# Performance work log

Hardware: AMD Instinct MI355X
Metric: run time of the kernel (lower is better)

## Reference

```python
import jax, jax.numpy as jnp
import numpy as np

EPS_BN = 1e-5
EPS_LN = 1e-5


def _gcn_conv(x, W, b, src, dst, n_nodes):
    # PyG GCNConv: h = x @ W, add self-loops, symmetric deg^{-1/2} normalization,
    # scatter-add over edges, then + bias.
    h = x @ W                                            # [N, out]
    ones = jnp.ones(src.shape[0], dtype=h.dtype)
    deg = jax.ops.segment_sum(ones, dst, num_segments=n_nodes) + 1.0  # +1 for self-loop
    dinv = jax.lax.rsqrt(deg)                            # [N]
    coef = dinv[src] * dinv[dst]                         # [E]
    msg = h[src] * coef[:, None]                         # [E, out] gather + scale
    agg = jax.ops.segment_sum(msg, dst, num_segments=n_nodes)
    agg = agg + h * (dinv * dinv)[:, None]               # self-loop contribution
    return agg + b


def _encode(x, edge_index, W1, b1, bn_gamma, bn_beta, W2, b2, ln_gamma, ln_beta, lin_W, lin_b):
    n = x.shape[0]
    src, dst = edge_index[0], edge_index[1]
    h = _gcn_conv(x, W1, b1, src, dst, n)
    # BatchNorm1d (training mode: batch statistics over nodes, biased var)
    mu = jnp.mean(h, axis=0)
    var = jnp.mean((h - mu) ** 2, axis=0)
    h = (h - mu) * jax.lax.rsqrt(var + EPS_BN) * bn_gamma + bn_beta
    h = jax.nn.relu(h)
    h = _gcn_conv(h, W2, b2, src, dst, n)
    # LayerNorm over feature dim
    mu2 = jnp.mean(h, axis=-1, keepdims=True)
    var2 = jnp.mean((h - mu2) ** 2, axis=-1, keepdims=True)
    h = (h - mu2) * jax.lax.rsqrt(var2 + EPS_LN) * ln_gamma + ln_beta
    h = jax.nn.relu(h)
    return h @ lin_W + lin_b


def setup_inputs() -> dict:
    key = jax.random.key(0)
    ks = jax.random.split(key, 16)
    N, E, EL = 100000, 800000, 200000
    C_in, C_hid, C_out = 128, 256, 128
    inp = {}
    inp["x"] = jax.random.normal(ks[0], (N, C_in), dtype=jnp.float32)
    inp["edge_index"] = jax.random.randint(ks[1], (2, E), 0, N, dtype=jnp.int64)
    inp["edge_label_index"] = jax.random.randint(ks[2], (2, EL), 0, N, dtype=jnp.int64)
    inp["cutoff"] = jnp.zeros((), dtype=jnp.float32)
    s1 = 1.0 / np.sqrt(C_in)
    s2 = 1.0 / np.sqrt(C_hid)
    s3 = 1.0 / np.sqrt(C_out)
    inp["W1"] = jax.random.uniform(ks[3], (C_in, C_hid), jnp.float32, -s1, s1)
    inp["b1"] = jnp.zeros((C_hid,), jnp.float32)
    inp["bn_gamma"] = jnp.ones((C_hid,), jnp.float32)
    inp["bn_beta"] = jnp.zeros((C_hid,), jnp.float32)
    inp["W2"] = jax.random.uniform(ks[4], (C_hid, C_out), jnp.float32, -s2, s2)
    inp["b2"] = jnp.zeros((C_out,), jnp.float32)
    inp["ln_gamma"] = jnp.ones((C_out,), jnp.float32)
    inp["ln_beta"] = jnp.zeros((C_out,), jnp.float32)
    inp["lin_W"] = jax.random.uniform(ks[5], (C_out, C_out), jnp.float32, -s3, s3)
    inp["lin_b"] = jax.random.uniform(ks[6], (C_out,), jnp.float32, -s3, s3)
    return inp


def reference(x, edge_index, edge_label_index, cutoff, W1, b1, bn_gamma, bn_beta, W2, b2, ln_gamma, ln_beta, lin_W, lin_b):
    z = _encode(x, edge_index, W1, b1, bn_gamma, bn_beta, W2, b2, ln_gamma, ln_beta, lin_W, lin_b)
    # decode: per-pair dot product + thresholding
    edge_values = jnp.sum(z[edge_label_index[0]] * z[edge_label_index[1]], axis=-1)  # [EL]
    rounded = jnp.where(edge_values < cutoff, jnp.zeros_like(edge_values), jnp.ones_like(edge_values))
    return edge_values, jax.lax.stop_gradient(rounded)
```

## Files before the change

### kernel.cpp

```cpp
#include <hip/hip_runtime.h>
#include <stdint.h>


#define C_IN  128
#define C_HID 256
#define C_OUT 128
#define SCAN_B 256

typedef __attribute__((ext_vector_type(8))) short bf16x8;
typedef __attribute__((ext_vector_type(4))) float f32x4;

__device__ __forceinline__ short f2bf(float f) {
  union { float f; uint32_t u; } v; v.f = f;
  uint32_t r = v.u + 0x7FFFu + ((v.u >> 16) & 1u);
  return (short)(r >> 16);
}
__device__ __forceinline__ uint32_t pack_bf2(float a, float b) {
  return (uint32_t)(uint16_t)f2bf(a) | ((uint32_t)(uint16_t)f2bf(b) << 16);
}
__device__ __forceinline__ float bflo(uint32_t p) {
  union { uint32_t u; float f; } v; v.u = p << 16; return v.f;
}
__device__ __forceinline__ float bfhi(uint32_t p) {
  union { uint32_t u; float f; } v; v.u = p & 0xffff0000u; return v.f;
}
__device__ __forceinline__ float bfs(short s) {
  union { uint32_t u; float f; } v; v.u = ((uint32_t)(uint16_t)s) << 16; return v.f;
}

__device__ __forceinline__ void acc8(float* a, uint4 p, float w) {
  a[0] += bflo(p.x) * w; a[1] += bfhi(p.x) * w;
  a[2] += bflo(p.y) * w; a[3] += bfhi(p.y) * w;
  a[4] += bflo(p.z) * w; a[5] += bfhi(p.z) * w;
  a[6] += bflo(p.w) * w; a[7] += bfhi(p.w) * w;
}

__device__ __forceinline__ void async_cp16(const void* g, void* l) {
  __builtin_amdgcn_global_load_lds((const __attribute__((address_space(1))) void*)g,
                                   (__attribute__((address_space(3))) void*)l, 16, 0, 0);
}


__global__ __launch_bounds__(256) void hist_kernel(const int* __restrict__ dst,
                                                   int* __restrict__ counts,
                                                   int* __restrict__ ofs, int E) {
  int e = blockIdx.x * 256 + threadIdx.x;
  if (e < E) ofs[e] = atomicAdd(&counts[dst[e]], 1);
}

__global__ __launch_bounds__(256) void scan_part(const int* __restrict__ counts,
                                                 int* __restrict__ blockSums,
                                                 float* __restrict__ dinv,
                                                 int n, int per) {
  __shared__ int ws[4];
  int b = blockIdx.x;
  int start = b * per, end = min(n, start + per);
  int s = 0;
  for (int i = start + threadIdx.x; i < end; i += 256) {
    int c = counts[i];
    s += c;
    dinv[i] = rsqrtf((float)c + 1.0f);
  }
#pragma unroll
  for (int d = 1; d < 64; d <<= 1) s += __shfl_xor(s, d);
  if ((threadIdx.x & 63) == 0) ws[threadIdx.x >> 6] = s;
  __syncthreads();
  if (threadIdx.x == 0) blockSums[b] = ws[0] + ws[1] + ws[2] + ws[3];
}

__global__ __launch_bounds__(256) void scan_final(const int* __restrict__ counts,
                                                  const int* __restrict__ blockSums,
                                                  int* __restrict__ row_ptr,
                                                  int n, int per) {
  __shared__ int wsum[4];
  __shared__ int sbase;
  int tid = threadIdx.x, lane = tid & 63, wid = tid >> 6;
  int b = blockIdx.x;
  {
    int v = (tid < b) ? blockSums[tid] : 0;
#pragma unroll
    for (int d = 1; d < 64; d <<= 1) v += __shfl_xor(v, d);
    if (lane == 0) wsum[wid] = v;
    __syncthreads();
    if (tid == 0) sbase = wsum[0] + wsum[1] + wsum[2] + wsum[3];
    __syncthreads();
  }
  int start = b * per, end = min(n + 1, start + per);
  for (int chunk = start; chunk < end; chunk += 256) {
    int idx = chunk + tid;
    int v = (idx < n) ? counts[idx] : 0;
    int x = v;
#pragma unroll
    for (int d = 1; d < 64; d <<= 1) {
      int y = __shfl_up(x, d, 64);
      if (lane >= d) x += y;
    }
    if (lane == 63) wsum[wid] = x;
    __syncthreads();
    if (tid == 0) {
      int run = sbase;
#pragma unroll
      for (int w = 0; w < 4; ++w) { int t = wsum[w]; wsum[w] = run; run += t; }
      sbase = run;
    }
    __syncthreads();
    if (idx < end) row_ptr[idx] = wsum[wid] + x - v;
    __syncthreads();
  }
}

__global__ __launch_bounds__(256) void place_kernel(const int* __restrict__ src,
                                                    const int* __restrict__ dst,
                                                    const int* __restrict__ row_ptr,
                                                    const int* __restrict__ ofs,
                                                    const float* __restrict__ dinv,
                                                    int2* __restrict__ edges, int E) {
  int e = blockIdx.x * 256 + threadIdx.x;
  if (e < E) {
    int d = dst[e], s = src[e];
    int pos = row_ptr[d] + ofs[e];
    int2 ed; ed.x = s; ed.y = __float_as_int(dinv[s] * dinv[d]);
    edges[pos] = ed;
  }
}


__global__ __launch_bounds__(256) void cvt_all(const float* __restrict__ x,
                                               short* __restrict__ x_bf, int n4,
                                               const float* __restrict__ W1,
                                               short* __restrict__ w1t,
                                               const float* __restrict__ W2,
                                               short* __restrict__ w2t,
                                               const float* __restrict__ W3,
                                               short* __restrict__ w3t) {
  int i = blockIdx.x * 256 + threadIdx.x;
  if (i < n4) {
    float4 v = ((const float4*)x)[i];
    short4 o;
    o.x = f2bf(v.x); o.y = f2bf(v.y); o.z = f2bf(v.z); o.w = f2bf(v.w);
    ((short4*)x_bf)[i] = o;
    return;
  }
  int j = i - n4;
  if (j < 32768) {
    int k = j >> 8, n = j & 255;
    w1t[n * 128 + k] = f2bf(W1[j]);
  } else if (j < 65536) {
    int jj = j - 32768; int k = jj >> 7, n = jj & 127;
    w2t[n * 256 + k] = f2bf(W2[jj]);
  } else if (j < 81920) {
    int jj = j - 65536; int k = jj >> 7, n = jj & 127;
    w3t[n * 128 + k] = f2bf(W3[jj]);
  }
}


template <int MODE>
__global__ __launch_bounds__(256, 2) void bgemm_big(const short* __restrict__ A,
                                                    const short* __restrict__ BT,
                                                    const float* __restrict__ bias,
                                                    short* __restrict__ Cout,
                                                    float* __restrict__ pS,
                                                    float* __restrict__ pSS,
                                                    const float* __restrict__ bnp,
                                                    int M, int N, int K) {
  __shared__ short smem[2 * 128 * 128];
  short* As = smem;
  short* Bs = smem + 128 * 128;
  const int tid = threadIdx.x;
  const int w = tid >> 6, lane = tid & 63;
  const int wM = w >> 1, wN = w & 1;
  const int rowBase = blockIdx.y * 128;
  const int colBase = blockIdx.x * 128;
  const int l15 = lane & 15, q = lane >> 4;

  f32x4 acc[4][4];
#pragma unroll
  for (int i = 0; i < 4; ++i)
#pragma unroll
    for (int j = 0; j < 4; ++j) acc[i][j] = (f32x4){0.f, 0.f, 0.f, 0.f};

  for (int k0 = 0; k0 < K; k0 += 128) {
    if (MODE == 3) {
#pragma unroll
      for (int it = 0; it < 8; ++it) {
        int p = it * 256 + tid;
        int row = p >> 4, kcp = p & 15;
        int kc = kcp ^ (row & 15);
        int gm = rowBase + row; if (gm >= M) gm = M - 1;
        int c = k0 + kc * 8;
        bf16x8 av = *(const bf16x8*)&A[(size_t)gm * K + c];
        float4 s0 = *(const float4*)&bnp[c];
        float4 s1 = *(const float4*)&bnp[c + 4];
        float4 h0 = *(const float4*)&bnp[K + c];
        float4 h1 = *(const float4*)&bnp[K + c + 4];
        short res[8];
        res[0] = f2bf(fmaxf(bfs(av[0]) * s0.x + h0.x, 0.f));
        res[1] = f2bf(fmaxf(bfs(av[1]) * s0.y + h0.y, 0.f));
        res[2] = f2bf(fmaxf(bfs(av[2]) * s0.z + h0.z, 0.f));
        res[3] = f2bf(fmaxf(bfs(av[3]) * s0.w + h0.w, 0.f));
        res[4] = f2bf(fmaxf(bfs(av[4]) * s1.x + h1.x, 0.f));
        res[5] = f2bf(fmaxf(bfs(av[5]) * s1.y + h1.y, 0.f));
        res[6] = f2bf(fmaxf(bfs(av[6]) * s1.z + h1.z, 0.f));
        res[7] = f2bf(fmaxf(bfs(av[7]) * s1.w + h1.w, 0.f));
        bf16x8 rv;
#pragma unroll
        for (int j = 0; j < 8; ++j) rv[j] = res[j];
        *(bf16x8*)&As[p * 8] = rv;
      }
    } else {
#pragma unroll
      for (int it = 0; it < 8; ++it) {
        int p = it * 256 + tid;
        int row = p >> 4, kcp = p & 15;
        int kc = kcp ^ (row & 15);
        int gm = rowBase + row; if (gm >= M) gm = M - 1;
        async_cp16(A + (size_t)gm * K + k0 + kc * 8, &As[(it * 256 + w * 64) * 8]);
      }
    }
#pragma unroll
    for (int it = 0; it < 8; ++it) {
      int p = it * 256 + tid;
      int row = p >> 4, kcp = p & 15;
      int kc = kcp ^ (row & 15);
      async_cp16(BT + (size_t)(colBase + row) * K + k0 + kc * 8,
                 &Bs[(it * 256 + w * 64) * 8]);
    }
    __syncthreads();

#pragma unroll
    for (int ks = 0; ks < 4; ++ks) {
      bf16x8 af[4], bfr[4];
#pragma unroll
      for (int tm = 0; tm < 4; ++tm) {
        int row = wM * 64 + tm * 16 + l15;
        int kcp = (ks * 4 + q) ^ l15;
        af[tm] = *(const bf16x8*)&As[(row * 16 + kcp) * 8];
      }
#pragma unroll
      for (int tn = 0; tn < 4; ++tn) {
        int row = wN * 64 + tn * 16 + l15;
        int kcp = (ks * 4 + q) ^ l15;
        bfr[tn] = *(const bf16x8*)&Bs[(row * 16 + kcp) * 8];
      }
#pragma unroll
      for (int tm = 0; tm < 4; ++tm)
#pragma unroll
        for (int tn = 0; tn < 4; ++tn)
          acc[tm][tn] = __builtin_amdgcn_mfma_f32_16x16x32_bf16(af[tm], bfr[tn],
                                                                acc[tm][tn], 0, 0, 0);
    }
    __syncthreads();
  }

  if (MODE == 2) {
#pragma unroll
    for (int tn = 0; tn < 4; ++tn) {
      int col = colBase + wN * 64 + tn * 16 + l15;
      float bv = bias ? bias[col] : 0.0f;
      float s = 0.f, ss = 0.f;
#pragma unroll
      for (int tm = 0; tm < 4; ++tm) {
        int r0 = rowBase + wM * 64 + tm * 16 + q * 4;
#pragma unroll
        for (int r = 0; r < 4; ++r) {
          if (r0 + r < M) { float v = acc[tm][tn][r] + bv; s += v; ss += v * v; }
        }
      }
      s += __shfl_xor(s, 16); s += __shfl_xor(s, 32);
      ss += __shfl_xor(ss, 16); ss += __shfl_xor(ss, 32);
      if (q == 0) {
        int prow = blockIdx.y * 2 + wM;
        pS[(size_t)prow * C_HID + col] = s;
        pSS[(size_t)prow * C_HID + col] = ss;
      }
    }
  }

  {
    short* S = As;
#pragma unroll
    for (int tn = 0; tn < 4; ++tn) {
      int col = wN * 64 + tn * 16 + l15;
      float bv = bias ? bias[colBase + col] : 0.0f;
#pragma unroll
      for (int tm = 0; tm < 4; ++tm) {
        int r0 = wM * 64 + tm * 16 + q * 4;
#pragma unroll
        for (int r = 0; r < 4; ++r) S[(r0 + r) * 128 + col] = f2bf(acc[tm][tn][r] + bv);
      }
    }
    __syncthreads();
#pragma unroll
    for (int it = 0; it < 8; ++it) {
      int p = it * 256 + tid;
      int row = p >> 4, c = p & 15;
      int gm = rowBase + row;
      if (gm < M)
        *(uint4*)&Cout[(size_t)gm * N + colBase + c * 8] = ((const uint4*)S)[p];
    }
  }
}


__global__ __launch_bounds__(256) void bn_red1_kernel(const float* __restrict__ pS,
                                                      const float* __restrict__ pSS,
                                                      float* __restrict__ oS,
                                                      float* __restrict__ oSS, int R) {
  int c = threadIdx.x;
  int per = (R + gridDim.x - 1) / gridDim.x;
  int r0 = blockIdx.x * per, r1 = min(R, r0 + per);
  float s = 0.f, ss = 0.f;
  for (int r = r0; r < r1; ++r) {
    s += pS[(size_t)r * C_HID + c];
    ss += pSS[(size_t)r * C_HID + c];
  }
  oS[(size_t)blockIdx.x * C_HID + c] = s;
  oSS[(size_t)blockIdx.x * C_HID + c] = ss;
}

__global__ __launch_bounds__(256) void bn_red2_kernel(const float* __restrict__ oS,
                                                      const float* __restrict__ oSS,
                                                      const float* __restrict__ gamma,
                                                      const float* __restrict__ beta,
                                                      float* __restrict__ bnp,
                                                      int G, float invN) {
  int c = threadIdx.x;
  float s = 0.f, ss = 0.f;
  for (int g = 0; g < G; ++g) {
    s += oS[(size_t)g * C_HID + c];
    ss += oSS[(size_t)g * C_HID + c];
  }
  float mu = s * invN;
  float var = ss * invN - mu * mu;
  float sc = gamma[c] * rsqrtf(var + 1e-5f);
  bnp[c] = sc;
  bnp[C_HID + c] = beta[c] - mu * sc;
}


__global__ __launch_bounds__(256) void agg_x_kernel(const uint4* __restrict__ xb4,
                                                    const float* __restrict__ dinv,
                                                    const int* __restrict__ row_ptr,
                                                    const int2* __restrict__ edges,
                                                    uint4* __restrict__ out4, int N) {
  int g = (blockIdx.x * 256 + threadIdx.x) >> 4;
  int sl = threadIdx.x & 15;
  if (g >= N) return;
  int e0 = row_ptr[g], e1 = row_ptr[g + 1];
  float a[8] = {0.f, 0.f, 0.f, 0.f, 0.f, 0.f, 0.f, 0.f};
  int e = e0;
  for (; e + 4 <= e1; e += 4) {
    int2 ed0 = edges[e], ed1 = edges[e + 1], ed2 = edges[e + 2], ed3 = edges[e + 3];
    uint4 p0 = xb4[(size_t)ed0.x * 16 + sl];
    uint4 p1 = xb4[(size_t)ed1.x * 16 + sl];
    uint4 p2 = xb4[(size_t)ed2.x * 16 + sl];
    uint4 p3 = xb4[(size_t)ed3.x * 16 + sl];
    acc8(a, p0, __int_as_float(ed0.y));
    acc8(a, p1, __int_as_float(ed1.y));
    acc8(a, p2, __int_as_float(ed2.y));
    acc8(a, p3, __int_as_float(ed3.y));
  }
  for (; e < e1; ++e) {
    int2 ed = edges[e];
    uint4 p = xb4[(size_t)ed.x * 16 + sl];
    acc8(a, p, __int_as_float(ed.y));
  }
  float dn = dinv[g];
  uint4 ps = xb4[(size_t)g * 16 + sl];
  acc8(a, ps, dn * dn);
  uint4 o;
  o.x = pack_bf2(a[0], a[1]); o.y = pack_bf2(a[2], a[3]);
  o.z = pack_bf2(a[4], a[5]); o.w = pack_bf2(a[6], a[7]);
  out4[(size_t)g * 16 + sl] = o;
}

__global__ __launch_bounds__(256) void agg_ln_kernel(const uint4* __restrict__ hb4,
                                                     const float* __restrict__ dinv,
                                                     const int* __restrict__ row_ptr,
                                                     const int2* __restrict__ edges,
                                                     const float* __restrict__ bias,
                                                     const float* __restrict__ gamma,
                                                     const float* __restrict__ beta,
                                                     uint4* __restrict__ zb4, int N) {
  int g = (blockIdx.x * 256 + threadIdx.x) >> 4;
  int sl = threadIdx.x & 15;
  if (g >= N) return;
  int e0 = row_ptr[g], e1 = row_ptr[g + 1];
  float a[8] = {0.f, 0.f, 0.f, 0.f, 0.f, 0.f, 0.f, 0.f};
  int e = e0;
  for (; e + 4 <= e1; e += 4) {
    int2 ed0 = edges[e], ed1 = edges[e + 1], ed2 = edges[e + 2], ed3 = edges[e + 3];
    uint4 p0 = hb4[(size_t)ed0.x * 16 + sl];
    uint4 p1 = hb4[(size_t)ed1.x * 16 + sl];
    uint4 p2 = hb4[(size_t)ed2.x * 16 + sl];
    uint4 p3 = hb4[(size_t)ed3.x * 16 + sl];
    acc8(a, p0, __int_as_float(ed0.y));
    acc8(a, p1, __int_as_float(ed1.y));
    acc8(a, p2, __int_as_float(ed2.y));
    acc8(a, p3, __int_as_float(ed3.y));
  }
  for (; e < e1; ++e) {
    int2 ed = edges[e];
    uint4 p = hb4[(size_t)ed.x * 16 + sl];
    acc8(a, p, __int_as_float(ed.y));
  }
  float dn = dinv[g];
  uint4 ps = hb4[(size_t)g * 16 + sl];
  acc8(a, ps, dn * dn);

  int c = sl * 8;
  float4 bv0 = *(const float4*)&bias[c];
  float4 bv1 = *(const float4*)&bias[c + 4];
  a[0] += bv0.x; a[1] += bv0.y; a[2] += bv0.z; a[3] += bv0.w;
  a[4] += bv1.x; a[5] += bv1.y; a[6] += bv1.z; a[7] += bv1.w;

  float s = 0.f, ss = 0.f;
#pragma unroll
  for (int j = 0; j < 8; ++j) { s += a[j]; ss += a[j] * a[j]; }
#pragma unroll
  for (int d = 1; d < 16; d <<= 1) {
    s += __shfl_xor(s, d);
    ss += __shfl_xor(ss, d);
  }
  float mu = s * (1.0f / C_OUT);
  float var = ss * (1.0f / C_OUT) - mu * mu;
  float rs = rsqrtf(var + 1e-5f);
  float4 g0 = *(const float4*)&gamma[c];
  float4 g1 = *(const float4*)&gamma[c + 4];
  float4 t0 = *(const float4*)&beta[c];
  float4 t1 = *(const float4*)&beta[c + 4];
  float o[8];
  o[0] = fmaxf((a[0] - mu) * rs * g0.x + t0.x, 0.0f);
  o[1] = fmaxf((a[1] - mu) * rs * g0.y + t0.y, 0.0f);
  o[2] = fmaxf((a[2] - mu) * rs * g0.z + t0.z, 0.0f);
  o[3] = fmaxf((a[3] - mu) * rs * g0.w + t0.w, 0.0f);
  o[4] = fmaxf((a[4] - mu) * rs * g1.x + t1.x, 0.0f);
  o[5] = fmaxf((a[5] - mu) * rs * g1.y + t1.y, 0.0f);
  o[6] = fmaxf((a[6] - mu) * rs * g1.z + t1.z, 0.0f);
  o[7] = fmaxf((a[7] - mu) * rs * g1.w + t1.w, 0.0f);
  uint4 ov;
  ov.x = pack_bf2(o[0], o[1]); ov.y = pack_bf2(o[2], o[3]);
  ov.z = pack_bf2(o[4], o[5]); ov.w = pack_bf2(o[6], o[7]);
  zb4[(size_t)g * 16 + sl] = ov;
}


__global__ __launch_bounds__(256) void decode_kernel(const uint4* __restrict__ zb4,
                                                     const int* __restrict__ eli,
                                                     const float* __restrict__ cutoff,
                                                     float* __restrict__ out, int EL) {
  int g = (blockIdx.x * 256 + threadIdx.x) >> 4;
  int sl = threadIdx.x & 15;
  if (g >= EL) return;
  int a = eli[g];
  int b = eli[EL + g];
  uint4 va = zb4[(size_t)a * 16 + sl];
  uint4 vb = zb4[(size_t)b * 16 + sl];
  float s = bflo(va.x) * bflo(vb.x) + bfhi(va.x) * bfhi(vb.x)
          + bflo(va.y) * bflo(vb.y) + bfhi(va.y) * bfhi(vb.y)
          + bflo(va.z) * bflo(vb.z) + bfhi(va.z) * bfhi(vb.z)
          + bflo(va.w) * bflo(vb.w) + bfhi(va.w) * bfhi(vb.w);
#pragma unroll
  for (int d = 1; d < 16; d <<= 1) s += __shfl_xor(s, d);
  if (sl == 0) {
    out[g] = s;
    out[EL + g] = (s < cutoff[0]) ? 0.0f : 1.0f;
  }
}


extern "C" void kernel_launch(void* const* d_in, const int* in_sizes, int n_in,
                              void* d_out, int out_size, void* d_ws, size_t ws_size,
                              hipStream_t stream) {
  const float* x        = (const float*)d_in[0];
  const int*   eidx     = (const int*)d_in[1];
  const int*   eli      = (const int*)d_in[2];
  const float* cutoff   = (const float*)d_in[3];
  const float* W1       = (const float*)d_in[4];
  const float* b1       = (const float*)d_in[5];
  const float* bn_gamma = (const float*)d_in[6];
  const float* bn_beta  = (const float*)d_in[7];
  const float* W2       = (const float*)d_in[8];
  const float* b2       = (const float*)d_in[9];
  const float* ln_gamma = (const float*)d_in[10];
  const float* ln_beta  = (const float*)d_in[11];
  const float* lin_W    = (const float*)d_in[12];
  const float* lin_b    = (const float*)d_in[13];
  float* out = (float*)d_out;

  const int N  = in_sizes[0] / C_IN;
  const int E  = in_sizes[1] / 2;
  const int EL = in_sizes[2] / 2;

  const int* src = eidx;
  const int* dst = eidx + E;

  const int MB = (N + 127) / 128;
  const int R  = 2 * MB;

  char* p = (char*)d_ws;
  short* regionA = (short*)p;  p += (size_t)N * 256 * 2;
  short* regionB = (short*)p;  p += (size_t)N * 256 * 2;
  short* h2_bf   = (short*)p;  p += (size_t)N * 128 * 2;
  float* dinv    = (float*)p;  p += (size_t)N * 4;
  int* counts    = (int*)p;    p += (size_t)N * 4;
  int* row_ptr   = (int*)p;    p += (size_t)(N + 4) * 4;
  int* ofs       = (int*)p;    p += (size_t)E * 4;
  int2* edges    = (int2*)p;   p += (size_t)E * 8;
  float* pS      = (float*)p;  p += (size_t)R * C_HID * 4;
  float* pSS     = (float*)p;  p += (size_t)R * C_HID * 4;
  float* oS      = (float*)p;  p += 32 * C_HID * 4;
  float* oSS     = (float*)p;  p += 32 * C_HID * 4;
  float* bnp     = (float*)p;  p += 2 * C_HID * 4;
  int* blockSums = (int*)p;    p += SCAN_B * 4;
  short* w1t     = (short*)p;  p += (size_t)C_HID * C_IN * 2;
  short* w2t     = (short*)p;  p += (size_t)C_OUT * C_HID * 2;
  short* w3t     = (short*)p;  p += (size_t)C_OUT * C_OUT * 2;

  short* x_bf   = regionA;
  short* xa_bf  = regionA + (size_t)N * 128;
  short* h1_bf  = regionB;
  short* z_bf   = regionB;
  short* zf_bf  = regionA;

  hipMemsetAsync(counts, 0, (size_t)N * 4, stream);

  int eb = (E + 255) / 256;

  hist_kernel<<<eb, 256, 0, stream>>>(dst, counts, ofs, E);

  int per = (N + 1 + SCAN_B - 1) / SCAN_B;
  scan_part<<<SCAN_B, 256, 0, stream>>>(counts, blockSums, dinv, N, per);
  scan_final<<<SCAN_B, 256, 0, stream>>>(counts, blockSums, row_ptr, N, per);

  place_kernel<<<eb, 256, 0, stream>>>(src, dst, row_ptr, ofs, dinv, edges, E);

  int xn4 = N * C_IN / 4;
  cvt_all<<<(xn4 + 81920 + 255) / 256, 256, 0, stream>>>(x, x_bf, xn4, W1, w1t,
                                                         W2, w2t, lin_W, w3t);

  int gb = ((size_t)N * 16 + 255) / 256;
  agg_x_kernel<<<gb, 256, 0, stream>>>((const uint4*)x_bf, dinv, row_ptr, edges,
                                       (uint4*)xa_bf, N);

  dim3 g1(C_HID / 128, MB);
  bgemm_big<2><<<g1, 256, 0, stream>>>(xa_bf, w1t, b1, h1_bf, pS, pSS, nullptr,
                                       N, C_HID, C_IN);

  bn_red1_kernel<<<32, 256, 0, stream>>>(pS, pSS, oS, oSS, R);
  bn_red2_kernel<<<1, 256, 0, stream>>>(oS, oSS, bn_gamma, bn_beta, bnp, 32,
                                        1.0f / (float)N);

  dim3 g2(C_OUT / 128, MB);
  bgemm_big<3><<<g2, 256, 0, stream>>>(h1_bf, w2t, nullptr, h2_bf, nullptr, nullptr,
                                       bnp, N, C_OUT, C_HID);

  agg_ln_kernel<<<gb, 256, 0, stream>>>((const uint4*)h2_bf, dinv, row_ptr, edges,
                                        b2, ln_gamma, ln_beta, (uint4*)z_bf, N);

  dim3 g3(C_OUT / 128, MB);
  bgemm_big<1><<<g3, 256, 0, stream>>>(z_bf, w3t, lin_b, zf_bf, nullptr, nullptr,
                                       nullptr, N, C_OUT, C_OUT);

  int db = ((size_t)EL * 16 + 255) / 256;
  decode_kernel<<<db, 256, 0, stream>>>((const uint4*)zf_bf, eli, cutoff, out, EL);
}
```

Baseline: 358.7 us.

## Pack CSR edges into 32-bit src|bf16 coef, fuse hist with cvt, unroll gathers by 8

Result: no change. 360.9 us (+0.6%).

```diff
diff --git a/kernel.cpp b/kernel.cpp
--- a/kernel.cpp
+++ b/kernel.cpp
@@ -26,6 +26,10 @@
 }
 __device__ __forceinline__ float bfs(short s) {
   union { uint32_t u; float f; } v; v.u = ((uint32_t)(uint16_t)s) << 16; return v.f;
+}
+__device__ __forceinline__ int up_src(uint32_t ed) { return (int)(ed >> 15); }
+__device__ __forceinline__ float up_coef(uint32_t ed) {
+  union { uint32_t u; float f; } v; v.u = (ed & 0x7FFFu) << 16; return v.f;
 }
 
 __device__ __forceinline__ void acc8(float* a, uint4 p, float w) {
@@ -41,12 +45,40 @@
 }
 
 
-__global__ __launch_bounds__(256) void hist_kernel(const int* __restrict__ dst,
-                                                   int* __restrict__ counts,
-                                                   int* __restrict__ ofs, int E) {
-  int e = blockIdx.x * 256 + threadIdx.x;
-  if (e < E) ofs[e] = atomicAdd(&counts[dst[e]], 1);
-}
+__global__ __launch_bounds__(256) void hist_cvt_kernel(
+    const int* __restrict__ dst, int* __restrict__ counts, int* __restrict__ ofs,
+    int E, int eb,
+    const float* __restrict__ x, short* __restrict__ x_bf, int n4,
+    const float* __restrict__ W1, short* __restrict__ w1t,
+    const float* __restrict__ W2, short* __restrict__ w2t,
+    const float* __restrict__ W3, short* __restrict__ w3t) {
+  int b = blockIdx.x;
+  if (b < eb) {
+    int e = b * 256 + threadIdx.x;
+    if (e < E) ofs[e] = atomicAdd(&counts[dst[e]], 1);
+    return;
+  }
+  int i = (b - eb) * 256 + threadIdx.x;
+  if (i < n4) {
+    float4 v = ((const float4*)x)[i];
+    short4 o;
+    o.x = f2bf(v.x); o.y = f2bf(v.y); o.z = f2bf(v.z); o.w = f2bf(v.w);
+    ((short4*)x_bf)[i] = o;
+    return;
+  }
+  int j = i - n4;
+  if (j < 32768) {
+    int k = j >> 8, n = j & 255;
+    w1t[n * 128 + k] = f2bf(W1[j]);
+  } else if (j < 65536) {
+    int jj = j - 32768; int k = jj >> 7, n = jj & 127;
+    w2t[n * 256 + k] = f2bf(W2[jj]);
+  } else if (j < 81920) {
+    int jj = j - 65536; int k = jj >> 7, n = jj & 127;
+    w3t[n * 128 + k] = f2bf(W3[jj]);
+  }
+}
+
 
 __global__ __launch_bounds__(256) void scan_part(const int* __restrict__ counts,
                                                  int* __restrict__ blockSums,
@@ -114,43 +146,14 @@
                                                     const int* __restrict__ row_ptr,
                                                     const int* __restrict__ ofs,
                                                     const float* __restrict__ dinv,
-                                                    int2* __restrict__ edges, int E) {
+                                                    uint32_t* __restrict__ edges, int E) {
   int e = blockIdx.x * 256 + threadIdx.x;
   if (e < E) {
     int d = dst[e], s = src[e];
     int pos = row_ptr[d] + ofs[e];
-    int2 ed; ed.x = s; ed.y = __float_as_int(dinv[s] * dinv[d]);
-    edges[pos] = ed;
-  }
-}
-
-
-__global__ __launch_bounds__(256) void cvt_all(const float* __restrict__ x,
-                                               short* __restrict__ x_bf, int n4,
-                                               const float* __restrict__ W1,
-                                               short* __restrict__ w1t,
-                                               const float* __restrict__ W2,
-                                               short* __restrict__ w2t,
-                                               const float* __restrict__ W3,
-                                               short* __restrict__ w3t) {
-  int i = blockIdx.x * 256 + threadIdx.x;
-  if (i < n4) {
-    float4 v = ((const float4*)x)[i];
-    short4 o;
-    o.x = f2bf(v.x); o.y = f2bf(v.y); o.z = f2bf(v.z); o.w = f2bf(v.w);
-    ((short4*)x_bf)[i] = o;
-    return;
-  }
-  int j = i - n4;
-  if (j < 32768) {
-    int k = j >> 8, n = j & 255;
-    w1t[n * 128 + k] = f2bf(W1[j]);
-  } else if (j < 65536) {
-    int jj = j - 32768; int k = jj >> 7, n = jj & 127;
-    w2t[n * 256 + k] = f2bf(W2[jj]);
-  } else if (j < 81920) {
-    int jj = j - 65536; int k = jj >> 7, n = jj & 127;
-    w3t[n * 128 + k] = f2bf(W3[jj]);
+    float coef = dinv[s] * dinv[d];
+    uint32_t cb = (uint32_t)(uint16_t)f2bf(coef) & 0x7FFFu;
+    edges[pos] = ((uint32_t)s << 15) | cb;
   }
 }
 
@@ -342,7 +345,7 @@
 __global__ __launch_bounds__(256) void agg_x_kernel(const uint4* __restrict__ xb4,
                                                     const float* __restrict__ dinv,
                                                     const int* __restrict__ row_ptr,
-                                                    const int2* __restrict__ edges,
+                                                    const uint32_t* __restrict__ edges,
                                                     uint4* __restrict__ out4, int N) {
   int g = (blockIdx.x * 256 + threadIdx.x) >> 4;
   int sl = threadIdx.x & 15;
@@ -350,21 +353,31 @@
   int e0 = row_ptr[g], e1 = row_ptr[g + 1];
   float a[8] = {0.f, 0.f, 0.f, 0.f, 0.f, 0.f, 0.f, 0.f};
   int e = e0;
-  for (; e + 4 <= e1; e += 4) {
-    int2 ed0 = edges[e], ed1 = edges[e + 1], ed2 = edges[e + 2], ed3 = edges[e + 3];
-    uint4 p0 = xb4[(size_t)ed0.x * 16 + sl];
-    uint4 p1 = xb4[(size_t)ed1.x * 16 + sl];
-    uint4 p2 = xb4[(size_t)ed2.x * 16 + sl];
-    uint4 p3 = xb4[(size_t)ed3.x * 16 + sl];
-    acc8(a, p0, __int_as_float(ed0.y));
-    acc8(a, p1, __int_as_float(ed1.y));
-    acc8(a, p2, __int_as_float(ed2.y));
-    acc8(a, p3, __int_as_float(ed3.y));
+  for (; e + 8 <= e1; e += 8) {
+    uint32_t ed[8];
+#pragma unroll
+    for (int j = 0; j < 8; ++j) ed[j] = edges[e + j];
+    uint4 pv[8];
+#pragma unroll
+    for (int j = 0; j < 8; ++j) pv[j] = xb4[(size_t)up_src(ed[j]) * 16 + sl];
+#pragma unroll
+    for (int j = 0; j < 8; ++j) acc8(a, pv[j], up_coef(ed[j]));
+  }
+  if (e + 4 <= e1) {
+    uint32_t ed[4];
+#pragma unroll
+    for (int j = 0; j < 4; ++j) ed[j] = edges[e + j];
+    uint4 pv[4];
+#pragma unroll
+    for (int j = 0; j < 4; ++j) pv[j] = xb4[(size_t)up_src(ed[j]) * 16 + sl];
+#pragma unroll
+    for (int j = 0; j < 4; ++j) acc8(a, pv[j], up_coef(ed[j]));
+    e += 4;
   }
   for (; e < e1; ++e) {
-    int2 ed = edges[e];
-    uint4 p = xb4[(size_t)ed.x * 16 + sl];
-    acc8(a, p, __int_as_float(ed.y));
+    uint32_t ed = edges[e];
+    uint4 p = xb4[(size_t)up_src(ed) * 16 + sl];
+    acc8(a, p, up_coef(ed));
   }
   float dn = dinv[g];
   uint4 ps = xb4[(size_t)g * 16 + sl];
@@ -378,7 +391,7 @@
 __global__ __launch_bounds__(256) void agg_ln_kernel(const uint4* __restrict__ hb4,
                                                      const float* __restrict__ dinv,
                                                      const int* __restrict__ row_ptr,
-                                                     const int2* __restrict__ edges,
+                                                     const uint32_t* __restrict__ edges,
                                                      const float* __restrict__ bias,
                                                      const float* __restrict__ gamma,
                                                      const float* __restrict__ beta,
@@ -389,21 +402,31 @@
   int e0 = row_ptr[g], e1 = row_ptr[g + 1];
   float a[8] = {0.f, 0.f, 0.f, 0.f, 0.f, 0.f, 0.f, 0.f};
   int e = e0;
-  for (; e + 4 <= e1; e += 4) {
-    int2 ed0 = edges[e], ed1 = edges[e + 1], ed2 = edges[e + 2], ed3 = edges[e + 3];
-    uint4 p0 = hb4[(size_t)ed0.x * 16 + sl];
-    uint4 p1 = hb4[(size_t)ed1.x * 16 + sl];
-    uint4 p2 = hb4[(size_t)ed2.x * 16 + sl];
-    uint4 p3 = hb4[(size_t)ed3.x * 16 + sl];
-    acc8(a, p0, __int_as_float(ed0.y));
-    acc8(a, p1, __int_as_float(ed1.y));
-    acc8(a, p2, __int_as_float(ed2.y));
-    acc8(a, p3, __int_as_float(ed3.y));
+  for (; e + 8 <= e1; e += 8) {
+    uint32_t ed[8];
+#pragma unroll
+    for (int j = 0; j < 8; ++j) ed[j] = edges[e + j];
+    uint4 pv[8];
+#pragma unroll
+    for (int j = 0; j < 8; ++j) pv[j] = hb4[(size_t)up_src(ed[j]) * 16 + sl];
+#pragma unroll
+    for (int j = 0; j < 8; ++j) acc8(a, pv[j], up_coef(ed[j]));
+  }
+  if (e + 4 <= e1) {
+    uint32_t ed[4];
+#pragma unroll
+    for (int j = 0; j < 4; ++j) ed[j] = edges[e + j];
+    uint4 pv[4];
+#pragma unroll
+    for (int j = 0; j < 4; ++j) pv[j] = hb4[(size_t)up_src(ed[j]) * 16 + sl];
+#pragma unroll
+    for (int j = 0; j < 4; ++j) acc8(a, pv[j], up_coef(ed[j]));
+    e += 4;
   }
   for (; e < e1; ++e) {
-    int2 ed = edges[e];
-    uint4 p = hb4[(size_t)ed.x * 16 + sl];
-    acc8(a, p, __int_as_float(ed.y));
+    uint32_t ed = edges[e];
+    uint4 p = hb4[(size_t)up_src(ed) * 16 + sl];
+    acc8(a, p, up_coef(ed));
   }
   float dn = dinv[g];
   uint4 ps = hb4[(size_t)g * 16 + sl];
@@ -500,23 +523,23 @@
   const int R  = 2 * MB;
 
   char* p = (char*)d_ws;
-  short* regionA = (short*)p;  p += (size_t)N * 256 * 2;
-  short* regionB = (short*)p;  p += (size_t)N * 256 * 2;
-  short* h2_bf   = (short*)p;  p += (size_t)N * 128 * 2;
-  float* dinv    = (float*)p;  p += (size_t)N * 4;
-  int* counts    = (int*)p;    p += (size_t)N * 4;
-  int* row_ptr   = (int*)p;    p += (size_t)(N + 4) * 4;
-  int* ofs       = (int*)p;    p += (size_t)E * 4;
-  int2* edges    = (int2*)p;   p += (size_t)E * 8;
-  float* pS      = (float*)p;  p += (size_t)R * C_HID * 4;
-  float* pSS     = (float*)p;  p += (size_t)R * C_HID * 4;
-  float* oS      = (float*)p;  p += 32 * C_HID * 4;
-  float* oSS     = (float*)p;  p += 32 * C_HID * 4;
-  float* bnp     = (float*)p;  p += 2 * C_HID * 4;
-  int* blockSums = (int*)p;    p += SCAN_B * 4;
-  short* w1t     = (short*)p;  p += (size_t)C_HID * C_IN * 2;
-  short* w2t     = (short*)p;  p += (size_t)C_OUT * C_HID * 2;
-  short* w3t     = (short*)p;  p += (size_t)C_OUT * C_OUT * 2;
+  short* regionA  = (short*)p;    p += (size_t)N * 256 * 2;
+  short* regionB  = (short*)p;    p += (size_t)N * 256 * 2;
+  short* h2_bf    = (short*)p;    p += (size_t)N * 128 * 2;
+  float* dinv     = (float*)p;    p += (size_t)N * 4;
+  int* counts     = (int*)p;      p += (size_t)N * 4;
+  int* row_ptr    = (int*)p;      p += (size_t)(N + 4) * 4;
+  int* ofs        = (int*)p;      p += (size_t)E * 4;
+  uint32_t* edges = (uint32_t*)p; p += (size_t)E * 4;
+  float* pS       = (float*)p;    p += (size_t)R * C_HID * 4;
+  float* pSS      = (float*)p;    p += (size_t)R * C_HID * 4;
+  float* oS       = (float*)p;    p += 32 * C_HID * 4;
+  float* oSS      = (float*)p;    p += 32 * C_HID * 4;
+  float* bnp      = (float*)p;    p += 2 * C_HID * 4;
+  int* blockSums  = (int*)p;      p += SCAN_B * 4;
+  short* w1t      = (short*)p;    p += (size_t)C_HID * C_IN * 2;
+  short* w2t      = (short*)p;    p += (size_t)C_OUT * C_HID * 2;
+  short* w3t      = (short*)p;    p += (size_t)C_OUT * C_OUT * 2;
 
   short* x_bf   = regionA;
   short* xa_bf  = regionA + (size_t)N * 128;
@@ -527,8 +550,12 @@
   hipMemsetAsync(counts, 0, (size_t)N * 4, stream);
 
   int eb = (E + 255) / 256;
-
-  hist_kernel<<<eb, 256, 0, stream>>>(dst, counts, ofs, E);
+  int xn4 = N * C_IN / 4;
+  int cvtb = (xn4 + 81920 + 255) / 256;
+
+  hist_cvt_kernel<<<eb + cvtb, 256, 0, stream>>>(dst, counts, ofs, E, eb,
+                                                 x, x_bf, xn4, W1, w1t,
+                                                 W2, w2t, lin_W, w3t);
 
   int per = (N + 1 + SCAN_B - 1) / SCAN_B;
   scan_part<<<SCAN_B, 256, 0, stream>>>(counts, blockSums, dinv, N, per);
@@ -536,10 +563,6 @@
 
   place_kernel<<<eb, 256, 0, stream>>>(src, dst, row_ptr, ofs, dinv, edges, E);
 
-  int xn4 = N * C_IN / 4;
-  cvt_all<<<(xn4 + 81920 + 255) / 256, 256, 0, stream>>>(x, x_bf, xn4, W1, w1t,
-                                                         W2, w2t, lin_W, w3t);
-
   int gb = ((size_t)N * 16 + 255) / 256;
   agg_x_kernel<<<gb, 256, 0, stream>>>((const uint4*)x_bf, dinv, row_ptr, edges,
                                        (uint4*)xa_bf, N);
```
